# Kernel tuning notes

Measured on AMD Instinct MI355X. Metric: run time of the kernel, lower is better.

The kernel has to match this reference:

```python
import jax, jax.numpy as jnp
import numpy as np

N_MET, N_RXN, D, C, H, E = 20000, 40000, 256, 64, 4, 250000
P = 0.2  # MC dropout prob (always active)


def setup_inputs() -> dict:
    key = jax.random.key(0)
    ks = jax.random.split(key, 40)
    g = lambda i, shape: jax.random.normal(ks[i], shape, jnp.float32) * 0.05
    inp = {
        'x_met': jax.random.normal(ks[0], (N_MET, D), jnp.float32),
        'x_rxn': jax.random.normal(ks[1], (N_RXN, D), jnp.float32),
        'sub_src': jax.random.randint(ks[2], (E,), 0, N_MET),
        'sub_dst': jax.random.randint(ks[3], (E,), 0, N_RXN),
        'prod_src': jax.random.randint(ks[4], (E,), 0, N_RXN),
        'prod_dst': jax.random.randint(ks[5], (E,), 0, N_MET),
        'shr_src': jax.random.randint(ks[6], (E,), 0, N_RXN),
        'shr_dst': jax.random.randint(ks[7], (E,), 0, N_RXN),
    }
    i = 8
    for name in ['sub', 'prod', 'shr']:
        inp['Wl_' + name] = g(i, (D, H * C)); inp['bl_' + name] = g(i + 1, (H * C,))
        inp['Wr_' + name] = g(i + 2, (D, H * C)); inp['br_' + name] = g(i + 3, (H * C,))
        inp['att_' + name] = g(i + 4, (H, C)); inp['b_' + name] = g(i + 5, (C,))
        i += 6
    inp['W_proj_rxn'] = g(26, (D, C)); inp['b_proj_rxn'] = g(27, (C,))
    inp['W_proj_met'] = g(28, (D, C)); inp['b_proj_met'] = g(29, (C,))
    inp['ln_rxn_g'] = jnp.ones((C,), jnp.float32); inp['ln_rxn_b'] = jnp.zeros((C,), jnp.float32)
    inp['ln_met_g'] = jnp.ones((C,), jnp.float32); inp['ln_met_b'] = jnp.zeros((C,), jnp.float32)
    return inp


def gatv2(xs, xd, src, dst, Wl, bl, Wr, br, att, bias, n_dst):
    # GATv2Conv (concat=False): mean over heads, eval-mode attention (no attn dropout).
    Hh, Cc = att.shape
    xl = (xs @ Wl + bl).reshape(xs.shape[0], Hh, Cc)  # source transform
    xr = (xd @ Wr + br).reshape(xd.shape[0], Hh, Cc)  # destination transform
    s = jax.nn.leaky_relu(xl[src] + xr[dst], 0.2)     # [E,H,C]
    e = jnp.einsum('ehc,hc->eh', s, att)              # [E,H] per-edge scores
    m = jax.ops.segment_max(e, dst, num_segments=n_dst)
    m = jnp.where(jnp.isfinite(m), m, 0.0)            # nodes with no in-edges
    ex = jnp.exp(e - m[dst])
    den = jax.ops.segment_sum(ex, dst, num_segments=n_dst)
    alpha = ex / (den[dst] + 1e-16)                   # segment softmax (PyG eps)
    out = jax.ops.segment_sum(alpha[:, :, None] * xl[src], dst, num_segments=n_dst)
    return out.mean(axis=1) + bias                    # [n_dst, C]


def layernorm(x, g, b):
    mu = x.mean(-1, keepdims=True)
    var = x.var(-1, keepdims=True)
    return (x - mu) * jax.lax.rsqrt(var + 1e-5) * g + b


def mc_dropout(x, key):
    mask = jax.random.bernoulli(key, 1.0 - P, x.shape)
    return jnp.where(mask, x / (1.0 - P), 0.0)


def reference(x_met, x_rxn, sub_src, sub_dst, prod_src, prod_dst, shr_src, shr_dst,
              Wl_sub, bl_sub, Wr_sub, br_sub, att_sub, b_sub,
              Wl_prod, bl_prod, Wr_prod, br_prod, att_prod, b_prod,
              Wl_shr, bl_shr, Wr_shr, br_shr, att_shr, b_shr,
              W_proj_rxn, b_proj_rxn, W_proj_met, b_proj_met,
              ln_rxn_g, ln_rxn_b, ln_met_g, ln_met_b):
    # shared_metabolite relation: add_self_loops=True
    sl = jnp.arange(N_RXN, dtype=shr_src.dtype)
    shr_src_f = jnp.concatenate([shr_src, sl])
    shr_dst_f = jnp.concatenate([shr_dst, sl])

    out_sub = gatv2(x_met, x_rxn, sub_src, sub_dst, Wl_sub, bl_sub, Wr_sub, br_sub, att_sub, b_sub, N_RXN)
    out_shr = gatv2(x_rxn, x_rxn, shr_src_f, shr_dst_f, Wl_shr, bl_shr, Wr_shr, br_shr, att_shr, b_shr, N_RXN)
    out_prod = gatv2(x_rxn, x_met, prod_src, prod_dst, Wl_prod, bl_prod, Wr_prod, br_prod, att_prod, b_prod, N_MET)

    rxn = 0.5 * (out_sub + out_shr)  # HeteroConv aggr='mean' over 2 relations
    met = out_prod                   # single relation -> mean is identity

    rxn = layernorm(jax.nn.elu(rxn) + (x_rxn @ W_proj_rxn + b_proj_rxn), ln_rxn_g, ln_rxn_b)
    met = layernorm(jax.nn.elu(met) + (x_met @ W_proj_met + b_proj_met), ln_met_g, ln_met_b)

    k1, k2 = jax.random.split(jax.random.key(1))
    return mc_dropout(rxn, k1), mc_dropout(met, k2)
```

## Files before the change

kernel.cpp:

```cpp
#include <hip/hip_runtime.h>
#include <hip/hip_bf16.h>
#include <stdint.h>

#define NMET 20000
#define NRXN 40000
#define DDIM 256
#define CDIM 64

typedef __attribute__((ext_vector_type(8))) short bf16x8;
typedef __attribute__((ext_vector_type(4))) float f32x4;

typedef __attribute__((address_space(1))) const void gvoid_t;
typedef __attribute__((address_space(3))) void lvoid_t;

__host__ __device__ inline void tf2x32(unsigned k0, unsigned k1,
                                       unsigned x0, unsigned x1,
                                       unsigned &o0, unsigned &o1) {
  unsigned ks2 = k0 ^ k1 ^ 0x1BD11BDAu;
#define TFR(r) { x0 += x1; x1 = (x1 << r) | (x1 >> (32 - r)); x1 ^= x0; }
  x0 += k0; x1 += k1;
  TFR(13) TFR(15) TFR(26) TFR(6)
  x0 += k1; x1 += ks2 + 1u;
  TFR(17) TFR(29) TFR(16) TFR(24)
  x0 += ks2; x1 += k0 + 2u;
  TFR(13) TFR(15) TFR(26) TFR(6)
  x0 += k0; x1 += k1 + 3u;
  TFR(17) TFR(29) TFR(16) TFR(24)
  x0 += k1; x1 += ks2 + 4u;
  TFR(13) TFR(15) TFR(26) TFR(6)
  x0 += ks2; x1 += k0 + 5u;
#undef TFR
  o0 = x0; o1 = x1;
}

__device__ inline unsigned short f2bbits(float f) {
  __hip_bfloat16 h = __float2bfloat16(f);
  return *reinterpret_cast<unsigned short*>(&h);
}
__device__ inline float b2f(unsigned short u) {
  unsigned v = (unsigned)u << 16;
  return __uint_as_float(v);
}

#define CVT_A_BLK 2500
#define CVT_B_BLK 5000
__global__ __launch_bounds__(256) void prep_all(
    const float* __restrict__ x_met, __hip_bfloat16* __restrict__ xmb,
    const float* __restrict__ x_rxn, __hip_bfloat16* __restrict__ xrb,
    const float* w0, const float* w1, const float* w2, const float* w3,
    const float* w4, const float* w5, const float* w6, const float* w7,
    __hip_bfloat16* o0, __hip_bfloat16* o1, __hip_bfloat16* o2, __hip_bfloat16* o3,
    __hip_bfloat16* o4, __hip_bfloat16* o5, __hip_bfloat16* o6, __hip_bfloat16* o7) {
  __shared__ float ts[32][33];
  int bid = blockIdx.x;
  if (bid < CVT_A_BLK + CVT_B_BLK) {
    const float* in; __hip_bfloat16* out; int n;
    if (bid < CVT_A_BLK) { in = x_met; out = xmb; n = NMET * DDIM; }
    else { in = x_rxn; out = xrb; n = NRXN * DDIM; bid -= CVT_A_BLK; }
    int i = (bid * 256 + threadIdx.x) * 8;
    if (i >= n) return;
    float4 va = *reinterpret_cast<const float4*>(in + i);
    float4 vb = *reinterpret_cast<const float4*>(in + i + 4);
    bf16x8 o;
    o[0] = (short)f2bbits(va.x); o[1] = (short)f2bbits(va.y);
    o[2] = (short)f2bbits(va.z); o[3] = (short)f2bbits(va.w);
    o[4] = (short)f2bbits(vb.x); o[5] = (short)f2bbits(vb.y);
    o[6] = (short)f2bbits(vb.z); o[7] = (short)f2bbits(vb.w);
    *reinterpret_cast<bf16x8*>(out + i) = o;
    return;
  }
  int t = bid - (CVT_A_BLK + CVT_B_BLK);
  int z = t >> 6, tt = t & 63;
  const float* w; __hip_bfloat16* o; int Ncols;
  switch (z) {
    case 0: w = w0; o = o0; Ncols = 256; break;
    case 1: w = w1; o = o1; Ncols = 256; break;
    case 2: w = w2; o = o2; Ncols = 256; break;
    case 3: w = w3; o = o3; Ncols = 256; break;
    case 4: w = w4; o = o4; Ncols = 256; break;
    case 5: w = w5; o = o5; Ncols = 256; break;
    case 6: w = w6; o = o6; Ncols = 64; break;
    default: w = w7; o = o7; Ncols = 64; break;
  }
  int ntile = Ncols / 32;
  if (tt >= ntile * 8) return;
  int tn = tt % ntile, tk = tt / ntile;
  int tx = threadIdx.x & 31, ty = threadIdx.x >> 5;
#pragma unroll
  for (int r = ty; r < 32; r += 8)
    ts[r][tx] = w[(size_t)(tk * 32 + r) * Ncols + tn * 32 + tx];
  __syncthreads();
#pragma unroll
  for (int r = ty; r < 32; r += 8)
    o[(size_t)(tn * 32 + r) * 256 + tk * 32 + tx] = __float2bfloat16(ts[tx][r]);
}

struct TDesc {
  const __hip_bfloat16* X;
  const __hip_bfloat16* W;
  const float* bias;
  __hip_bfloat16* Yb;
  float* Yf;
  int M, N, nt, blocks;
};
struct TD8 { TDesc g[8]; };

__global__ __launch_bounds__(256) void gemm_tiled8(TD8 gd, int ng, int total) {
  __shared__ __align__(16) char As[16384];
  __shared__ __align__(16) char Bs[16384];
  int b = blockIdx.x;
  int q = total >> 3, r = total & 7;
  int xcd = b & 7, idx = b >> 3;
  int bid = (xcd < r) ? (xcd * (q + 1) + idx)
                      : (r * (q + 1) + (xcd - r) * q + idx);
  int di = 0;
  while (di < ng && bid >= gd.g[di].blocks) { bid -= gd.g[di].blocks; ++di; }
  if (di >= ng) return;
  TDesc g = gd.g[di];
  int mrow = bid / g.nt, ntile = bid - mrow * g.nt;
  int m0 = mrow * 128, n0 = ntile * 128;
  int tid = threadIdx.x, wave = tid >> 6, lane = tid & 63;
  int lr = lane & 15, lk = lane >> 4;
  int wm = wave >> 1, wn = wave & 1;
  int brows = g.N - n0; if (brows > 128) brows = 128;
  int bch = brows >> 3;
  int lrow = lane >> 3;
  int gsw = ((lane & 7) ^ lrow) * 8;

  f32x4 acc[4][4] = {};
  for (int kt = 0; kt < 4; ++kt) {
    for (int c = wave; c < 16; c += 4) {
      int row = m0 + c * 8 + lrow;
      if (row > g.M - 1) row = g.M - 1;
      const void* src = g.X + (size_t)row * DDIM + kt * 64 + gsw;
      __builtin_amdgcn_global_load_lds((gvoid_t*)src, (lvoid_t*)(As + c * 1024), 16, 0, 0);
    }
    for (int c = wave; c < bch; c += 4) {
      int row = n0 + c * 8 + lrow;
      const void* src = g.W + (size_t)row * DDIM + kt * 64 + gsw;
      __builtin_amdgcn_global_load_lds((gvoid_t*)src, (lvoid_t*)(Bs + c * 1024), 16, 0, 0);
    }
    __syncthreads();
#pragma unroll
    for (int kk = 0; kk < 2; ++kk) {
      bf16x8 a[4], b2[4];
#pragma unroll
      for (int m = 0; m < 4; ++m) {
        int row = wm * 64 + m * 16 + lr;
        int grp = (kk * 4 + lk) ^ (lr & 7);
        a[m] = *reinterpret_cast<const bf16x8*>(As + row * 128 + grp * 16);
      }
#pragma unroll
      for (int n = 0; n < 4; ++n) {
        int row = wn * 64 + n * 16 + lr;
        int grp = (kk * 4 + lk) ^ (lr & 7);
        b2[n] = *reinterpret_cast<const bf16x8*>(Bs + row * 128 + grp * 16);
      }
#pragma unroll
      for (int m = 0; m < 4; ++m)
#pragma unroll
        for (int n = 0; n < 4; ++n)
          acc[m][n] = __builtin_amdgcn_mfma_f32_16x16x32_bf16(a[m], b2[n], acc[m][n], 0, 0, 0);
    }
    __syncthreads();
  }
  bool isb = (g.Yb != nullptr);
#pragma unroll
  for (int m = 0; m < 4; ++m) {
#pragma unroll
    for (int rr = 0; rr < 4; ++rr) {
      int row = m0 + wm * 64 + m * 16 + lk * 4 + rr;
      if (row >= g.M) continue;
#pragma unroll
      for (int n = 0; n < 4; ++n) {
        int cg = n0 + wn * 64 + n * 16 + lr;
        if (cg >= g.N) continue;
        float v = acc[m][n][rr] + g.bias[cg];
        if (isb) g.Yb[(size_t)row * g.N + cg] = __float2bfloat16(v);
        else     g.Yf[(size_t)row * g.N + cg] = v;
      }
    }
  }
}

__global__ __launch_bounds__(256) void hist3(
    const int* __restrict__ d0, const int* __restrict__ d1, const int* __restrict__ d2,
    int E, int* __restrict__ c0, int* __restrict__ c1, int* __restrict__ c2) {
  int i = blockIdx.x * 256 + threadIdx.x;
  if (i >= E) return;
  int rel = blockIdx.y;
  if (rel == 0) atomicAdd(&c0[d0[i]], 1);
  else if (rel == 1) atomicAdd(&c1[d1[i]], 1);
  else atomicAdd(&c2[d2[i]], 1);
}

__global__ __launch_bounds__(256) void alloc3(
    const int* __restrict__ c0, const int* __restrict__ c1, const int* __restrict__ c2,
    int* __restrict__ o0, int* __restrict__ o1, int* __restrict__ o2,
    int* __restrict__ u0, int* __restrict__ u1, int* __restrict__ u2,
    int* __restrict__ cursors, int n0, int n1, int n2) {
  int rel = blockIdx.y;
  int i = blockIdx.x * 256 + threadIdx.x;
  const int* c = (rel == 0) ? c0 : (rel == 1) ? c1 : c2;
  int* o = (rel == 0) ? o0 : (rel == 1) ? o1 : o2;
  int* u = (rel == 0) ? u0 : (rel == 1) ? u1 : u2;
  int n = (rel == 0) ? n0 : (rel == 1) ? n1 : n2;
  if (i >= n) return;
  int cc = c[i];
  int pos = atomicAdd(&cursors[rel], cc);
  o[i] = pos; u[i] = pos;
}

__global__ __launch_bounds__(256) void scatter3(
    const int* __restrict__ s0, const int* __restrict__ d0,
    const int* __restrict__ s1, const int* __restrict__ d1,
    const int* __restrict__ s2, const int* __restrict__ d2,
    int E, int* __restrict__ u0, int* __restrict__ u1, int* __restrict__ u2,
    int* __restrict__ e0, int* __restrict__ e1, int* __restrict__ e2) {
  int i = blockIdx.x * 256 + threadIdx.x;
  if (i >= E) return;
  int rel = blockIdx.y;
  if (rel == 0)      { int pos = atomicAdd(&u0[d0[i]], 1); e0[pos] = s0[i]; }
  else if (rel == 1) { int pos = atomicAdd(&u1[d1[i]], 1); e1[pos] = s1[i]; }
  else               { int pos = atomicAdd(&u2[d2[i]], 1); e2[pos] = s2[i]; }
}

struct GatRel {
  const __hip_bfloat16* xl;
  const __hip_bfloat16* xr;
  const int* off; const int* cnt; const int* srce;
  const float* att; float* acc;
  int n; int self_loop;
};

__device__ inline float gat_wave(const GatRel& r, int d, int lane) {
  ushort4 ur = *reinterpret_cast<const ushort4*>(r.xr + (size_t)d * DDIM + 4 * lane);
  float c0 = b2f(ur.x), c1 = b2f(ur.y), c2 = b2f(ur.z), c3 = b2f(ur.w);
  float4 at = *reinterpret_cast<const float4*>(r.att + 4 * lane);

  float den = 0.f;
  float a0 = 0.f, a1 = 0.f, a2 = 0.f, a3 = 0.f;

#define EBODY(ux) {                                                             \
    float x0 = b2f(ux.x), x1 = b2f(ux.y), x2 = b2f(ux.z), x3 = b2f(ux.w);       \
    float t0 = x0 + c0; t0 = fmaxf(t0, 0.2f * t0);                              \
    float t1 = x1 + c1; t1 = fmaxf(t1, 0.2f * t1);                              \
    float t2 = x2 + c2; t2 = fmaxf(t2, 0.2f * t2);                              \
    float t3 = x3 + c3; t3 = fmaxf(t3, 0.2f * t3);                              \
    float pp = t0 * at.x + t1 * at.y + t2 * at.z + t3 * at.w;                   \
    pp += __shfl_xor(pp, 1); pp += __shfl_xor(pp, 2);                           \
    pp += __shfl_xor(pp, 4); pp += __shfl_xor(pp, 8);                           \
    float ex = __expf(pp);                                                      \
    den += ex;                                                                  \
    a0 = fmaf(ex, x0, a0); a1 = fmaf(ex, x1, a1);                               \
    a2 = fmaf(ex, x2, a2); a3 = fmaf(ex, x3, a3);                               \
  }
#define ELOAD(s_) *reinterpret_cast<const ushort4*>(r.xl + (size_t)(s_) * DDIM + 4 * lane)

  if (r.self_loop) { ushort4 ux = ELOAD(d); EBODY(ux) }
  int cnt = r.cnt[d];
  int beg = r.off[d];
  for (int jb = 0; jb < cnt; jb += 64) {
    int jj = jb + lane; if (jj > cnt - 1) jj = cnt - 1;
    int srcv = r.srce[beg + jj];
    int lim = cnt - jb; if (lim > 64) lim = 64;
    int u = 0;
    for (; u + 4 <= lim; u += 4) {
      int s0 = __shfl(srcv, u), s1 = __shfl(srcv, u + 1);
      int s2 = __shfl(srcv, u + 2), s3 = __shfl(srcv, u + 3);
      ushort4 ux0 = ELOAD(s0); ushort4 ux1 = ELOAD(s1);
      ushort4 ux2 = ELOAD(s2); ushort4 ux3 = ELOAD(s3);
      EBODY(ux0) EBODY(ux1) EBODY(ux2) EBODY(ux3)
    }
    for (; u < lim; ++u) {
      int s = __shfl(srcv, u);
      ushort4 ux = ELOAD(s); EBODY(ux)
    }
  }
#undef EBODY
#undef ELOAD

  float inv = (den > 0.f) ? 1.0f / den : 0.f;
  float p0 = a0 * inv, p1 = a1 * inv, p2 = a2 * inv, p3 = a3 * inv;
  p0 += __shfl_xor(p0, 16); p0 += __shfl_xor(p0, 32);
  p1 += __shfl_xor(p1, 16); p1 += __shfl_xor(p1, 32);
  p2 += __shfl_xor(p2, 16); p2 += __shfl_xor(p2, 32);
  p3 += __shfl_xor(p3, 16); p3 += __shfl_xor(p3, 32);
  int srcl = lane >> 2;
  float v0 = __shfl(p0, srcl);
  float v1 = __shfl(p1, srcl);
  float v2 = __shfl(p2, srcl);
  float v3 = __shfl(p3, srcl);
  float val = (lane & 2) ? ((lane & 1) ? v3 : v2) : ((lane & 1) ? v1 : v0);
  return 0.25f * val;
}

struct FDesc {
  const float* accA; const float* accB;
  float* out;
  const float* bA; const float* bB; float scale;
  const float* g; const float* be;
  int n; unsigned key0, key1;
};

__device__ inline void finalize_wave(const FDesc& f, int d, int lane, float agg) {
  unsigned idx = (unsigned)d * 64u + (unsigned)lane;
  float bias = f.bA[lane] + (f.bB ? f.bB[lane] : 0.f);
  float pre = f.scale * (agg + bias);
  pre = (pre > 0.f) ? pre : expm1f(pre);
  pre += f.out[idx];
  float mu = pre;
#pragma unroll
  for (int off = 32; off; off >>= 1) mu += __shfl_xor(mu, off);
  mu *= (1.0f / 64.0f);
  float dv = pre - mu;
  float var = dv * dv;
#pragma unroll
  for (int off = 32; off; off >>= 1) var += __shfl_xor(var, off);
  var *= (1.0f / 64.0f);
  float y = dv * rsqrtf(var + 1e-5f) * f.g[lane] + f.be[lane];
  unsigned o0, o1;
  tf2x32(f.key0, f.key1, 0u, idx, o0, o1);
  unsigned bits = o0 ^ o1;
  float u = __uint_as_float((bits >> 9) | 0x3f800000u) - 1.0f;
  y = (u < 0.8f) ? y / 0.8f : 0.0f;
  f.out[idx] = y;
}

__global__ __launch_bounds__(256) void gat_fused(
    GatRel rsub, GatRel rshr, GatRel rprod,
    FDesc frxn, FDesc fmet, int rxnBlocks) {
  __shared__ float lv[4][64];
  int wave = threadIdx.x >> 6, lane = threadIdx.x & 63;
  if (blockIdx.x < rxnBlocks) {
    int d = blockIdx.x * 2 + (wave >> 1);
    const GatRel& r = (wave & 1) ? rshr : rsub;
    float val = 0.f;
    if (d < rsub.n) val = gat_wave(r, d, lane);
    lv[wave][lane] = val;
    __syncthreads();
    if ((wave & 1) == 0 && d < rsub.n) {
      float agg = lv[wave][lane] + lv[wave + 1][lane];
      finalize_wave(frxn, d, lane, agg);
    }
  } else {
    int d = (blockIdx.x - rxnBlocks) * 4 + wave;
    if (d >= rprod.n) return;
    float agg = gat_wave(rprod, d, lane);
    finalize_wave(fmet, d, lane, agg);
  }
}

__global__ __launch_bounds__(256) void gat3(GatRel r0, GatRel r1, GatRel r2) {
  int gidx = blockIdx.x * 4 + (threadIdx.x >> 6);
  int lane = threadIdx.x & 63;
  GatRel r; int d;
  if (gidx < r0.n) { r = r0; d = gidx; }
  else if (gidx < r0.n + r1.n) { r = r1; d = gidx - r0.n; }
  else if (gidx < r0.n + r1.n + r2.n) { r = r2; d = gidx - r0.n - r1.n; }
  else return;
  r.acc[(size_t)d * 64 + lane] = gat_wave(r, d, lane);
}

__global__ __launch_bounds__(256) void finalize2(FDesc f0, FDesc f1) {
  int gidx = blockIdx.x * 4 + (threadIdx.x >> 6);
  int lane = threadIdx.x & 63;
  FDesc f; int d;
  if (gidx < f0.n) { f = f0; d = gidx; }
  else if (gidx < f0.n + f1.n) { f = f1; d = gidx - f0.n; }
  else return;
  unsigned idx = (unsigned)d * 64u + (unsigned)lane;
  float agg = f.accA[idx] + (f.accB ? f.accB[idx] : 0.f);
  finalize_wave(f, d, lane, agg);
}

extern "C" void kernel_launch(void* const* d_in, const int* in_sizes, int n_in,
                              void* d_out, int out_size, void* d_ws, size_t ws_size,
                              hipStream_t stream) {
  const float* x_met = (const float*)d_in[0];
  const float* x_rxn = (const float*)d_in[1];
  const int* sub_src = (const int*)d_in[2];
  const int* sub_dst = (const int*)d_in[3];
  const int* prod_src = (const int*)d_in[4];
  const int* prod_dst = (const int*)d_in[5];
  const int* shr_src = (const int*)d_in[6];
  const int* shr_dst = (const int*)d_in[7];
  const float* Wl_sub = (const float*)d_in[8];
  const float* bl_sub = (const float*)d_in[9];
  const float* Wr_sub = (const float*)d_in[10];
  const float* br_sub = (const float*)d_in[11];
  const float* att_sub = (const float*)d_in[12];
  const float* b_sub = (const float*)d_in[13];
  const float* Wl_prod = (const float*)d_in[14];
  const float* bl_prod = (const float*)d_in[15];
  const float* Wr_prod = (const float*)d_in[16];
  const float* br_prod = (const float*)d_in[17];
  const float* att_prod = (const float*)d_in[18];
  const float* b_prod = (const float*)d_in[19];
  const float* Wl_shr = (const float*)d_in[20];
  const float* bl_shr = (const float*)d_in[21];
  const float* Wr_shr = (const float*)d_in[22];
  const float* br_shr = (const float*)d_in[23];
  const float* att_shr = (const float*)d_in[24];
  const float* b_shr = (const float*)d_in[25];
  const float* W_proj_rxn = (const float*)d_in[26];
  const float* b_proj_rxn = (const float*)d_in[27];
  const float* W_proj_met = (const float*)d_in[28];
  const float* b_proj_met = (const float*)d_in[29];
  const float* ln_rxn_g = (const float*)d_in[30];
  const float* ln_rxn_b = (const float*)d_in[31];
  const float* ln_met_g = (const float*)d_in[32];
  const float* ln_met_b = (const float*)d_in[33];

  const int E = in_sizes[2];

  char* p = (char*)d_ws;
  auto take = [&](size_t b) { char* q = p; p += (b + 255) & ~(size_t)255; return q; };
  __hip_bfloat16* xmb = (__hip_bfloat16*)take((size_t)NMET * DDIM * 2);
  __hip_bfloat16* xrb = (__hip_bfloat16*)take((size_t)NRXN * DDIM * 2);
  __hip_bfloat16* wt[8];
  for (int i = 0; i < 6; ++i) wt[i] = (__hip_bfloat16*)take(256 * 256 * 2);
  for (int i = 6; i < 8; ++i) wt[i] = (__hip_bfloat16*)take(64 * 256 * 2);
  float* acc_sub = (float*)take((size_t)NRXN * CDIM * 4);
  float* acc_shr = (float*)take((size_t)NRXN * CDIM * 4);
  float* acc_met = (float*)take((size_t)NMET * CDIM * 4);
  int* cnt_sub = (int*)take((size_t)NRXN * 4 + (size_t)NRXN * 4 + (size_t)NMET * 4 + 16);
  int* cnt_shr = cnt_sub + NRXN;
  int* cnt_prod = cnt_shr + NRXN;
  int* cursors = cnt_prod + NMET;
  int* off_sub = (int*)take((size_t)NRXN * 4);
  int* off_shr = (int*)take((size_t)NRXN * 4);
  int* off_prod = (int*)take((size_t)NMET * 4);
  int* cur_sub = (int*)take((size_t)NRXN * 4);
  int* cur_shr = (int*)take((size_t)NRXN * 4);
  int* cur_prod = (int*)take((size_t)NMET * 4);
  int* srce_sub = (int*)take((size_t)E * 4);
  int* srce_shr = (int*)take((size_t)E * 4);
  int* srce_prod = (int*)take((size_t)E * 4);

  size_t met_b = (size_t)NMET * DDIM * 2, rxn_b = (size_t)NRXN * DDIM * 2;
  size_t used = (size_t)(p - (char*)d_ws);
  bool big = (ws_size >= used + 3 * met_b + 3 * rxn_b + 4096);

  __hip_bfloat16 *xl_sub, *xr_sub, *xl_shr, *xr_shr, *xl_prod, *xr_prod;
  if (big) {
    xl_sub = (__hip_bfloat16*)take(met_b);
    xr_sub = (__hip_bfloat16*)take(rxn_b);
    xl_shr = (__hip_bfloat16*)take(rxn_b);
    xr_shr = (__hip_bfloat16*)take(rxn_b);
    xl_prod = (__hip_bfloat16*)take(rxn_b);
    xr_prod = (__hip_bfloat16*)take(met_b);
  } else {
    __hip_bfloat16* xa = (__hip_bfloat16*)take(rxn_b);
    __hip_bfloat16* xb = (__hip_bfloat16*)take(rxn_b);
    xl_sub = xl_shr = xl_prod = xa;
    xr_sub = xr_shr = xr_prod = xb;
  }

  float* out_rxn = (float*)d_out;
  float* out_met = out_rxn + (size_t)NRXN * CDIM;

  unsigned k1_0, k1_1, k2_0, k2_1;
  tf2x32(0u, 1u, 0u, 0u, k1_0, k1_1);
  tf2x32(0u, 1u, 0u, 1u, k2_0, k2_1);

  dim3 blk(256);

  hipMemsetAsync(cnt_sub, 0, ((size_t)(NRXN + NRXN + NMET) + 4) * 4, stream);
  hist3<<<dim3((E + 255) / 256, 3), blk, 0, stream>>>(
      sub_dst, shr_dst, prod_dst, E, cnt_sub, cnt_shr, cnt_prod);
  alloc3<<<dim3((NRXN + 255) / 256, 3), blk, 0, stream>>>(
      cnt_sub, cnt_shr, cnt_prod, off_sub, off_shr, off_prod,
      cur_sub, cur_shr, cur_prod, cursors, NRXN, NRXN, NMET);
  prep_all<<<CVT_A_BLK + CVT_B_BLK + 512, blk, 0, stream>>>(
      x_met, xmb, x_rxn, xrb,
      Wl_sub, Wr_sub, Wl_shr, Wr_shr, Wl_prod, Wr_prod, W_proj_rxn, W_proj_met,
      wt[0], wt[1], wt[2], wt[3], wt[4], wt[5], wt[6], wt[7]);
  scatter3<<<dim3((E + 255) / 256, 3), blk, 0, stream>>>(
      sub_src, sub_dst, shr_src, shr_dst, prod_src, prod_dst, E,
      cur_sub, cur_shr, cur_prod, srce_sub, srce_shr, srce_prod);

  auto mk = [](const __hip_bfloat16* X, const __hip_bfloat16* W, const float* bias,
               __hip_bfloat16* Yb, float* Yf, int M, int N) {
    TDesc g; g.X = X; g.W = W; g.bias = bias; g.Yb = Yb; g.Yf = Yf;
    g.M = M; g.N = N; g.nt = (N + 127) / 128;
    g.blocks = ((M + 127) / 128) * g.nt;
    return g;
  };
  auto mkrel = [](const __hip_bfloat16* xl, const __hip_bfloat16* xr,
                  const int* off, const int* cnt, const int* srce,
                  const float* att, float* acc, int n, int sl) {
    GatRel r; r.xl = xl; r.xr = xr; r.off = off; r.cnt = cnt; r.srce = srce;
    r.att = att; r.acc = acc; r.n = n; r.self_loop = sl;
    return r;
  };
  GatRel rz{}; rz.n = 0;

  TDesc dsub_r  = mk(xrb, wt[1], br_sub,     xr_sub,  nullptr, NRXN, DDIM);
  TDesc dshr_l  = mk(xrb, wt[2], bl_shr,     xl_shr,  nullptr, NRXN, DDIM);
  TDesc dshr_r  = mk(xrb, wt[3], br_shr,     xr_shr,  nullptr, NRXN, DDIM);
  TDesc dprod_l = mk(xrb, wt[4], bl_prod,    xl_prod, nullptr, NRXN, DDIM);
  TDesc dproj_r = mk(xrb, wt[6], b_proj_rxn, nullptr, out_rxn, NRXN, CDIM);
  TDesc dsub_l  = mk(xmb, wt[0], bl_sub,     xl_sub,  nullptr, NMET, DDIM);
  TDesc dprod_m = mk(xmb, wt[5], br_prod,    xr_prod, nullptr, NMET, DDIM);
  TDesc dproj_m = mk(xmb, wt[7], b_proj_met, nullptr, out_met, NMET, CDIM);

  GatRel rsub = mkrel(xl_sub, xr_sub, off_sub, cnt_sub, srce_sub, att_sub, acc_sub, NRXN, 0);
  GatRel rshr = mkrel(xl_shr, xr_shr, off_shr, cnt_shr, srce_shr, att_shr, acc_shr, NRXN, 1);
  GatRel rprod = mkrel(xl_prod, xr_prod, off_prod, cnt_prod, srce_prod, att_prod, acc_met, NMET, 0);

  FDesc f0, f1;
  f0.accA = acc_sub; f0.accB = acc_shr; f0.out = out_rxn;
  f0.bA = b_sub; f0.bB = b_shr; f0.scale = 0.5f;
  f0.g = ln_rxn_g; f0.be = ln_rxn_b; f0.n = NRXN; f0.key0 = k1_0; f0.key1 = k1_1;
  f1.accA = acc_met; f1.accB = nullptr; f1.out = out_met;
  f1.bA = b_prod; f1.bB = nullptr; f1.scale = 1.0f;
  f1.g = ln_met_g; f1.be = ln_met_b; f1.n = NMET; f1.key0 = k2_0; f1.key1 = k2_1;

  if (big) {
    TD8 gd = {{dsub_r, dshr_l, dshr_r, dprod_l, dproj_r, dsub_l, dprod_m, dproj_m}};
    int tot = 0;
    for (int i = 0; i < 8; ++i) tot += gd.g[i].blocks;
    gemm_tiled8<<<tot, blk, 0, stream>>>(gd, 8, tot);
    int rxnBlocks = (NRXN + 1) / 2;
    int metBlocks = (NMET + 3) / 4;
    gat_fused<<<rxnBlocks + metBlocks, blk, 0, stream>>>(
        rsub, rshr, rprod, f0, f1, rxnBlocks);
  } else {
    TD8 gd1 = {{dproj_r, dproj_m, dsub_l, dsub_r}};
    int t1 = gd1.g[0].blocks + gd1.g[1].blocks + gd1.g[2].blocks + gd1.g[3].blocks;
    gemm_tiled8<<<t1, blk, 0, stream>>>(gd1, 4, t1);
    gat3<<<(NRXN + 3) / 4, blk, 0, stream>>>(rsub, rz, rz);
    TD8 gd2 = {{dshr_l, dshr_r}};
    int t2 = gd2.g[0].blocks + gd2.g[1].blocks;
    gemm_tiled8<<<t2, blk, 0, stream>>>(gd2, 2, t2);
    gat3<<<(NRXN + 3) / 4, blk, 0, stream>>>(rshr, rz, rz);
    TD8 gd3 = {{dprod_l, dprod_m}};
    int t3 = gd3.g[0].blocks + gd3.g[1].blocks;
    gemm_tiled8<<<t3, blk, 0, stream>>>(gd3, 2, t3);
    gat3<<<(NMET + 3) / 4, blk, 0, stream>>>(rprod, rz, rz);
    finalize2<<<(NRXN + NMET + 3) / 4, blk, 0, stream>>>(f0, f1);
  }
}
```

Measured before the change: 331.7 us.

## Process two edges per wave with 16-byte bf16x8 loads per lane in GATv2 aggregation

The per-destination GAT wave now splits into two half-waves, each handling a different source edge. Each lane loads 8 bf16 features (16 bytes) instead of 4, so the per-head dot product needs one fewer shuffle and the loop runs half as many iterations. Partial sums from the two halves are combined with xor-32 shuffles and the result is written through shared memory. In exchange it needs masking for odd edge counts and self-loops, more registers per lane, and an extra LDS round trip for the output.

```diff
diff --git a/kernel.cpp b/kernel.cpp
--- a/kernel.cpp
+++ b/kernel.cpp
@@ -233,31 +233,47 @@
   int n; int self_loop;
 };
 
-__device__ inline float gat_wave(const GatRel& r, int d, int lane) {
-  ushort4 ur = *reinterpret_cast<const ushort4*>(r.xr + (size_t)d * DDIM + 4 * lane);
-  float c0 = b2f(ur.x), c1 = b2f(ur.y), c2 = b2f(ur.z), c3 = b2f(ur.w);
-  float4 at = *reinterpret_cast<const float4*>(r.att + 4 * lane);
+__device__ inline void gat_wave2(const GatRel& r, int d, int lane,
+                                 float* __restrict__ lvout) {
+  int half = lane >> 5;
+  int il = lane & 31;
+  int foff = (il >> 3) * 64 + (il & 7) * 8;
+
+  bf16x8 urv = *reinterpret_cast<const bf16x8*>(r.xr + (size_t)d * DDIM + foff);
+  float cc[8];
+#pragma unroll
+  for (int j = 0; j < 8; ++j) cc[j] = b2f((unsigned short)urv[j]);
+  float4 atlo = *reinterpret_cast<const float4*>(r.att + foff);
+  float4 athi = *reinterpret_cast<const float4*>(r.att + foff + 4);
+  float at[8] = {atlo.x, atlo.y, atlo.z, atlo.w, athi.x, athi.y, athi.z, athi.w};
 
   float den = 0.f;
-  float a0 = 0.f, a1 = 0.f, a2 = 0.f, a3 = 0.f;
-
-#define EBODY(ux) {                                                             \
-    float x0 = b2f(ux.x), x1 = b2f(ux.y), x2 = b2f(ux.z), x3 = b2f(ux.w);       \
-    float t0 = x0 + c0; t0 = fmaxf(t0, 0.2f * t0);                              \
-    float t1 = x1 + c1; t1 = fmaxf(t1, 0.2f * t1);                              \
-    float t2 = x2 + c2; t2 = fmaxf(t2, 0.2f * t2);                              \
-    float t3 = x3 + c3; t3 = fmaxf(t3, 0.2f * t3);                              \
-    float pp = t0 * at.x + t1 * at.y + t2 * at.z + t3 * at.w;                   \
-    pp += __shfl_xor(pp, 1); pp += __shfl_xor(pp, 2);                           \
-    pp += __shfl_xor(pp, 4); pp += __shfl_xor(pp, 8);                           \
-    float ex = __expf(pp);                                                      \
-    den += ex;                                                                  \
-    a0 = fmaf(ex, x0, a0); a1 = fmaf(ex, x1, a1);                               \
-    a2 = fmaf(ex, x2, a2); a3 = fmaf(ex, x3, a3);                               \
-  }
-#define ELOAD(s_) *reinterpret_cast<const ushort4*>(r.xl + (size_t)(s_) * DDIM + 4 * lane)
-
-  if (r.self_loop) { ushort4 ux = ELOAD(d); EBODY(ux) }
+  float a[8] = {};
+
+#define PBODY(uxv, maskb) {                                          \
+    float pp = 0.f; float xx[8];                                     \
+    _Pragma("unroll")                                                \
+    for (int j = 0; j < 8; ++j) {                                    \
+      xx[j] = b2f((unsigned short)uxv[j]);                           \
+      float t = xx[j] + cc[j];                                       \
+      t = fmaxf(t, 0.2f * t);                                        \
+      pp = fmaf(t, at[j], pp);                                       \
+    }                                                                \
+    pp += __shfl_xor(pp, 1); pp += __shfl_xor(pp, 2);                \
+    pp += __shfl_xor(pp, 4);                                         \
+    float ex = __expf(pp);                                           \
+    if (maskb) ex = 0.f;                                             \
+    den += ex;                                                       \
+    _Pragma("unroll")                                                \
+    for (int j = 0; j < 8; ++j) a[j] = fmaf(ex, xx[j], a[j]);        \
+  }
+#define ELOAD(s_) *reinterpret_cast<const bf16x8*>(r.xl + (size_t)(s_) * DDIM + foff)
+
+  if (r.self_loop) {
+    bf16x8 ux = ELOAD(d);
+    bool mk = (half != 0);
+    PBODY(ux, mk)
+  }
   int cnt = r.cnt[d];
   int beg = r.off[d];
   for (int jb = 0; jb < cnt; jb += 64) {
@@ -266,33 +282,44 @@
     int lim = cnt - jb; if (lim > 64) lim = 64;
     int u = 0;
     for (; u + 4 <= lim; u += 4) {
-      int s0 = __shfl(srcv, u), s1 = __shfl(srcv, u + 1);
-      int s2 = __shfl(srcv, u + 2), s3 = __shfl(srcv, u + 3);
-      ushort4 ux0 = ELOAD(s0); ushort4 ux1 = ELOAD(s1);
-      ushort4 ux2 = ELOAD(s2); ushort4 ux3 = ELOAD(s3);
-      EBODY(ux0) EBODY(ux1) EBODY(ux2) EBODY(ux3)
-    }
-    for (; u < lim; ++u) {
-      int s = __shfl(srcv, u);
-      ushort4 ux = ELOAD(s); EBODY(ux)
-    }
-  }
-#undef EBODY
+      int sa0 = __shfl(srcv, u),     sb0 = __shfl(srcv, u + 1);
+      int sa1 = __shfl(srcv, u + 2), sb1 = __shfl(srcv, u + 3);
+      int s0 = half ? sb0 : sa0;
+      int s1 = half ? sb1 : sa1;
+      bf16x8 ux0 = ELOAD(s0); bf16x8 ux1 = ELOAD(s1);
+      PBODY(ux0, false) PBODY(ux1, false)
+    }
+    for (; u + 2 <= lim; u += 2) {
+      int sa = __shfl(srcv, u), sb = __shfl(srcv, u + 1);
+      int s = half ? sb : sa;
+      bf16x8 ux = ELOAD(s);
+      PBODY(ux, false)
+    }
+    if (u < lim) {
+      int sa = __shfl(srcv, u);
+      bf16x8 ux = ELOAD(sa);
+      bool mk = (half != 0);
+      PBODY(ux, mk)
+    }
+  }
+#undef PBODY
 #undef ELOAD
 
+  den += __shfl_xor(den, 32);
+#pragma unroll
+  for (int j = 0; j < 8; ++j) a[j] += __shfl_xor(a[j], 32);
   float inv = (den > 0.f) ? 1.0f / den : 0.f;
-  float p0 = a0 * inv, p1 = a1 * inv, p2 = a2 * inv, p3 = a3 * inv;
-  p0 += __shfl_xor(p0, 16); p0 += __shfl_xor(p0, 32);
-  p1 += __shfl_xor(p1, 16); p1 += __shfl_xor(p1, 32);
-  p2 += __shfl_xor(p2, 16); p2 += __shfl_xor(p2, 32);
-  p3 += __shfl_xor(p3, 16); p3 += __shfl_xor(p3, 32);
-  int srcl = lane >> 2;
-  float v0 = __shfl(p0, srcl);
-  float v1 = __shfl(p1, srcl);
-  float v2 = __shfl(p2, srcl);
-  float v3 = __shfl(p3, srcl);
-  float val = (lane & 2) ? ((lane & 1) ? v3 : v2) : ((lane & 1) ? v1 : v0);
-  return 0.25f * val;
+#pragma unroll
+  for (int j = 0; j < 8; ++j) {
+    float v = a[j] * inv;
+    v += __shfl_xor(v, 8);
+    v += __shfl_xor(v, 16);
+    a[j] = 0.25f * v;
+  }
+  if (lane < 8) {
+#pragma unroll
+    for (int j = 0; j < 8; ++j) lvout[lane * 8 + j] = a[j];
+  }
 }
 
 struct FDesc {
@@ -335,9 +362,7 @@
   if (blockIdx.x < rxnBlocks) {
     int d = blockIdx.x * 2 + (wave >> 1);
     const GatRel& r = (wave & 1) ? rshr : rsub;
-    float val = 0.f;
-    if (d < rsub.n) val = gat_wave(r, d, lane);
-    lv[wave][lane] = val;
+    if (d < rsub.n) gat_wave2(r, d, lane, lv[wave]);
     __syncthreads();
     if ((wave & 1) == 0 && d < rsub.n) {
       float agg = lv[wave][lane] + lv[wave + 1][lane];
@@ -346,20 +371,24 @@
   } else {
     int d = (blockIdx.x - rxnBlocks) * 4 + wave;
     if (d >= rprod.n) return;
-    float agg = gat_wave(rprod, d, lane);
+    gat_wave2(rprod, d, lane, lv[wave]);
+    float agg = lv[wave][lane];
     finalize_wave(fmet, d, lane, agg);
   }
 }
 
 __global__ __launch_bounds__(256) void gat3(GatRel r0, GatRel r1, GatRel r2) {
-  int gidx = blockIdx.x * 4 + (threadIdx.x >> 6);
+  __shared__ float lv[4][64];
+  int wave = threadIdx.x >> 6;
+  int gidx = blockIdx.x * 4 + wave;
   int lane = threadIdx.x & 63;
   GatRel r; int d;
   if (gidx < r0.n) { r = r0; d = gidx; }
   else if (gidx < r0.n + r1.n) { r = r1; d = gidx - r0.n; }
   else if (gidx < r0.n + r1.n + r2.n) { r = r2; d = gidx - r0.n - r1.n; }
   else return;
-  r.acc[(size_t)d * 64 + lane] = gat_wave(r, d, lane);
+  gat_wave2(r, d, lane, lv[wave]);
+  r.acc[(size_t)d * 64 + lane] = lv[wave][lane];
 }
 
 __global__ __launch_bounds__(256) void finalize2(FDesc f0, FDesc f1) {
```

Measured after the change: 345.3 us. +4.1%, slower.
